# Performance work log

Hardware: AMD Instinct MI355X
Metric: run time of the kernel (lower is better)

The kernel has to match this reference:

```python
import jax, jax.numpy as jnp
import numpy as np

N, E, F_IN, D_HID, H, N_CLS = 50000, 800000, 128, 96, 8, 40
DH = D_HID // H  # 12
NEG_SLOPE = 0.2


def setup_inputs() -> dict:
    key = jax.random.key(0)
    ks = jax.random.split(key, 14)
    x = jax.random.normal(ks[0], (N, F_IN), dtype=jnp.float32)
    edge_src = jax.random.randint(ks[1], (E,), 0, N, dtype=jnp.int32)
    edge_dst = jax.random.randint(ks[2], (E,), 0, N, dtype=jnp.int32)
    s = 0.1  # keep attention logits in a stable range
    W0 = jax.random.normal(ks[3], (F_IN, D_HID), dtype=jnp.float32) * s
    as0 = jax.random.normal(ks[4], (H, DH), dtype=jnp.float32) * s
    ad0 = jax.random.normal(ks[5], (H, DH), dtype=jnp.float32) * s
    b0 = jnp.zeros((D_HID,), dtype=jnp.float32)
    W1 = jax.random.normal(ks[6], (D_HID, D_HID), dtype=jnp.float32) * s
    as1 = jax.random.normal(ks[7], (H, DH), dtype=jnp.float32) * s
    ad1 = jax.random.normal(ks[8], (H, DH), dtype=jnp.float32) * s
    b1 = jnp.zeros((D_HID,), dtype=jnp.float32)
    Wout = jax.random.normal(ks[9], (D_HID, N_CLS), dtype=jnp.float32) * s
    bout = jnp.zeros((N_CLS,), dtype=jnp.float32)
    return dict(x=x, edge_src=edge_src, edge_dst=edge_dst, W0=W0, as0=as0,
                ad0=ad0, b0=b0, W1=W1, as1=as1, ad1=ad1, b1=b1,
                Wout=Wout, bout=bout)


def _gat_conv(x, src, dst, W, a_src, a_dst, b):
    """PyG-style GATConv: per-head linear, edge attention, segment softmax, scatter-sum."""
    n = x.shape[0]
    h = (x @ W).reshape(n, H, DH)                       # [N, H, Dh]
    alpha_s = jnp.einsum('nhd,hd->nh', h, a_src)        # [N, H]
    alpha_d = jnp.einsum('nhd,hd->nh', h, a_dst)        # [N, H]
    e = alpha_s[src] + alpha_d[dst]                     # [E, H]
    e = jnp.where(e > 0, e, NEG_SLOPE * e)              # LeakyReLU(0.2)
    # numerically-stable segment softmax over edges grouped by destination
    m = jax.ops.segment_max(e, dst, num_segments=n)     # [N, H]
    m = jnp.where(jnp.isfinite(m), m, 0.0)
    p = jnp.exp(e - m[dst])                             # [E, H]
    z = jax.ops.segment_sum(p, dst, num_segments=n)     # [N, H]
    alpha = p / (z[dst] + 1e-16)                        # [E, H]
    msg = h[src] * alpha[:, :, None]                    # [E, H, Dh]
    out = jax.ops.segment_sum(msg, dst, num_segments=n) # [N, H, Dh]
    return out.reshape(n, H * DH) + b


def reference(x, edge_src, edge_dst, W0, as0, ad0, b0, W1, as1, ad1, b1, Wout, bout):
    src = edge_src.astype(jnp.int32)
    dst = edge_dst.astype(jnp.int32)
    h = _gat_conv(x, src, dst, W0, as0, ad0, b0)                 # input_fc (no activation)
    h = jax.nn.relu(_gat_conv(h, src, dst, W1, as1, ad1, b1))    # conv layer + ReLU (eval: no dropout)
    out = h @ Wout + bout
    return jax.nn.log_softmax(out, axis=1)
```

## Files before the change

kernel.cpp:

```cpp
#include <hip/hip_runtime.h>
#include <hip/hip_fp16.h>
#include <math.h>

#define N_NODES 50000
#define N_EDGES 800000
#define F_IN    128
#define D_HID   96
#define NHEAD   8
#define DH      12
#define N_CLS   40
#define NEG_SLOPE 0.2f

#define NPART   (N_NODES / 8)
#define CKS     64
#define CHK     (N_EDGES / CKS)
#define NHB     (8 * CKS)

#define GBM 64
#define NGB ((N_NODES + GBM - 1) / GBM)
#define WPAD 136

#define HALFN   (N_NODES / 2)
#define AGG_NPB 32
#define NAGGB   ((HALFN + AGG_NPB - 1) / AGG_NPB)

typedef _Float16 f16x8 __attribute__((ext_vector_type(8)));
typedef float    f32x4 __attribute__((ext_vector_type(4)));

__global__ __launch_bounds__(256) void pre_kernel(
    const float* __restrict__ W0, const float* __restrict__ W1,
    _Float16* __restrict__ wt0, _Float16* __restrict__ wt1)
{
    int b = blockIdx.x, t = threadIdx.x;
    if (b < 48) {
        int idx = b * 256 + t;
        int n = idx >> 7, k = idx & 127;
        wt0[idx] = (_Float16)W0[k * D_HID + n];
    } else {
        int idx = (b - 48) * 256 + t;
        int n = idx / 96, k = idx - n * 96;
        wt1[idx] = (_Float16)W1[k * D_HID + n];
    }
}

template<bool A16>
__device__ __forceinline__ void gemm_alpha_mfma_body(
    const void* __restrict__ Av, const _Float16* __restrict__ WT,
    const float* __restrict__ asrc, const float* __restrict__ adst,
    uint4* __restrict__ Hrec,
    int M, int K, int bid,
    _Float16 (*Wt)[WPAD], _Float16 (*Hl)[104], float* avl, float* adl)
{
    int tid  = threadIdx.x;
    int lane = tid & 63;
    int w    = tid >> 6;
    int n0   = bid * GBM;

    int cpr = K >> 3;
    int nch = 96 * cpr;
    for (int ch = tid; ch < nch; ch += 256) {
        int row = ch / cpr, off = (ch - row * cpr) << 3;
        *(f16x8*)&Wt[row][off] = *(const f16x8*)&WT[row * K + off];
    }
    if (tid < 96) { avl[tid] = asrc[tid]; adl[tid] = adst[tid]; }
    __syncthreads();

    int c  = lane & 15;
    int kg = lane >> 4;
    int arow = n0 + (w << 4) + c;
    int ar = arow < M ? arow : M - 1;

    f32x4 acc[6];
#pragma unroll
    for (int t = 0; t < 6; t++) acc[t] = (f32x4){0.f, 0.f, 0.f, 0.f};

    for (int k0 = 0; k0 < K; k0 += 32) {
        f16x8 av;
        if constexpr (A16) {
            const _Float16* ap = (const _Float16*)Av + (size_t)ar * K + (kg << 3);
            av = *(const f16x8*)(ap + k0);
        } else {
            const float* ap = (const float*)Av + (size_t)ar * K + (kg << 3);
            float4 a0 = *(const float4*)(ap + k0);
            float4 a1 = *(const float4*)(ap + k0 + 4);
            av[0] = (_Float16)a0.x; av[1] = (_Float16)a0.y;
            av[2] = (_Float16)a0.z; av[3] = (_Float16)a0.w;
            av[4] = (_Float16)a1.x; av[5] = (_Float16)a1.y;
            av[6] = (_Float16)a1.z; av[7] = (_Float16)a1.w;
        }
#pragma unroll
        for (int t = 0; t < 6; t++) {
            f16x8 bv = *(const f16x8*)&Wt[t * 16 + c][k0 + (kg << 3)];
            acc[t] = __builtin_amdgcn_mfma_f32_16x16x32_f16(av, bv, acc[t], 0, 0, 0);
        }
    }

    int rbase = (w << 4) + (kg << 2);
#pragma unroll
    for (int t = 0; t < 6; t++)
#pragma unroll
        for (int r = 0; r < 4; r++)
            Hl[rbase + r][t * 16 + c] = (_Float16)acc[t][r];
    __syncthreads();

    int row = tid >> 2, q = tid & 3;
    int gr = n0 + row;
    if (gr < M) {
        float s0 = 0.f, s1 = 0.f, d0 = 0.f, d1 = 0.f;
#pragma unroll
        for (int j = 0; j < 12; j++) {
            float f = (float)Hl[row][q * 24 + j];
            s0 += f * avl[q * 24 + j];
            d0 += f * adl[q * 24 + j];
        }
#pragma unroll
        for (int j = 12; j < 24; j++) {
            float f = (float)Hl[row][q * 24 + j];
            s1 += f * avl[q * 24 + j];
            d1 += f * adl[q * 24 + j];
        }
        const uint* hp = (const uint*)&Hl[row][q * 24];
        uint4* rec = Hrec + ((size_t)q * N_NODES + gr) * 4;
        rec[0] = make_uint4(__float_as_uint(s0), hp[0], hp[1], hp[2]);
        rec[1] = make_uint4(hp[3], hp[4], hp[5], __float_as_uint(d0));
        rec[2] = make_uint4(__float_as_uint(s1), hp[6], hp[7], hp[8]);
        rec[3] = make_uint4(hp[9], hp[10], hp[11], __float_as_uint(d1));
    }
}

__global__ __launch_bounds__(256) void hist_gemm_kernel(
    const int* __restrict__ edst, unsigned short* __restrict__ Hmat,
    const float* __restrict__ A, const _Float16* __restrict__ WT,
    const float* __restrict__ asrc, const float* __restrict__ adst,
    uint4* __restrict__ Hrec)
{
    __shared__ __align__(16) char smem[40448];
    if (blockIdx.x < NHB) {
        int* lh = (int*)smem;
        int g = blockIdx.x & 7, c = blockIdx.x >> 3;
        int lo = g * NPART;
        for (int i = threadIdx.x; i < NPART; i += 256) lh[i] = 0;
        __syncthreads();
        const int4* d4 = (const int4*)(edst + c * CHK);
        for (int i = threadIdx.x; i < CHK / 4; i += 256) {
            int4 dv = d4[i];
            int a = dv.x - lo, b = dv.y - lo, cc = dv.z - lo, dd = dv.w - lo;
            if ((unsigned)a  < (unsigned)NPART) atomicAdd(&lh[a], 1);
            if ((unsigned)b  < (unsigned)NPART) atomicAdd(&lh[b], 1);
            if ((unsigned)cc < (unsigned)NPART) atomicAdd(&lh[cc], 1);
            if ((unsigned)dd < (unsigned)NPART) atomicAdd(&lh[dd], 1);
        }
        __syncthreads();
        unsigned int* hrow = (unsigned int*)(Hmat + (size_t)c * N_NODES + lo);
        for (int i = threadIdx.x; i < NPART / 2; i += 256)
            hrow[i] = (unsigned)lh[2 * i] | ((unsigned)lh[2 * i + 1] << 16);
    } else {
        _Float16 (*Wt)[WPAD] = (_Float16(*)[WPAD])smem;
        _Float16 (*Hl)[104]  = (_Float16(*)[104])(smem + 26112);
        float* avl = (float*)(smem + 26112 + 13312);
        float* adl = avl + 96;
        gemm_alpha_mfma_body<false>(A, WT, asrc, adst, Hrec, N_NODES, F_IN,
                                    blockIdx.x - NHB, Wt, Hl, avl, adl);
    }
}

__global__ __launch_bounds__(256) void gemm_alpha_kernel(
    const _Float16* __restrict__ A, const _Float16* __restrict__ WT,
    const float* __restrict__ asrc, const float* __restrict__ adst,
    uint4* __restrict__ Hrec, int M, int K)
{
    __shared__ __align__(16) char smem[40448];
    _Float16 (*Wt)[WPAD] = (_Float16(*)[WPAD])smem;
    _Float16 (*Hl)[104]  = (_Float16(*)[104])(smem + 26112);
    float* avl = (float*)(smem + 26112 + 13312);
    float* adl = avl + 96;
    gemm_alpha_mfma_body<true>(A, WT, asrc, adst, Hrec, M, K, blockIdx.x,
                               Wt, Hl, avl, adl);
}

__global__ void scan1_kernel(const unsigned short* __restrict__ Hmat,
                             int* __restrict__ cnt, int* __restrict__ incl,
                             int* __restrict__ partials, int n) {
    __shared__ int sdata[256];
    int t = threadIdx.x;
    int base = blockIdx.x * 1024 + t * 4;
    int v[4] = {0, 0, 0, 0};
    if (base + 4 <= n) {
        for (int c = 0; c < CKS; c++) {
            ushort4 h = *(const ushort4*)&Hmat[(size_t)c * N_NODES + base];
            v[0] += h.x; v[1] += h.y; v[2] += h.z; v[3] += h.w;
        }
    } else if (base < n) {
        for (int c = 0; c < CKS; c++)
#pragma unroll
            for (int j = 0; j < 4; j++)
                if (base + j < n) v[j] += Hmat[(size_t)c * N_NODES + base + j];
    }
#pragma unroll
    for (int j = 0; j < 4; j++) if (base + j < n) cnt[base + j] = v[j];
    v[1] += v[0]; v[2] += v[1]; v[3] += v[2];
    sdata[t] = v[3];
    __syncthreads();
    for (int off = 1; off < 256; off <<= 1) {
        int x = (t >= off) ? sdata[t - off] : 0;
        __syncthreads();
        sdata[t] += x;
        __syncthreads();
    }
    int excl = sdata[t] - v[3];
#pragma unroll
    for (int j = 0; j < 4; j++) { int i = base + j; if (i < n) incl[i] = v[j] + excl; }
    if (t == 255) partials[blockIdx.x] = sdata[255];
}

__global__ void scan3_kernel(const int* __restrict__ cnt, const int* __restrict__ incl,
                             const int* __restrict__ partials,
                             const unsigned short* __restrict__ Hmat,
                             int* __restrict__ Bmat, int* __restrict__ rowptr,
                             int n, int nb) {
    int i = blockIdx.x * blockDim.x + threadIdx.x;
    if (i >= n) return;
    int myb = i >> 10;
    int psum = 0;
    for (int b = 0; b < nb; b++) psum += (b < myb) ? partials[b] : 0;
    int v = incl[i] + psum;
    rowptr[i + 1] = v;
    if (i == 0) rowptr[0] = 0;
    int running = v - cnt[i];
    for (int c = 0; c < CKS; c++) {
        Bmat[(size_t)c * N_NODES + i] = running;
        running += Hmat[(size_t)c * N_NODES + i];
    }
}

__global__ __launch_bounds__(256) void fill_kernel(
    const int* __restrict__ esrc, const int* __restrict__ edst,
    const int* __restrict__ Bmat, unsigned short* __restrict__ srclist)
{
    __shared__ int cur[NPART];
    int g = blockIdx.x & 7, c = blockIdx.x >> 3;
    int lo = g * NPART;
    const int* brow = Bmat + (size_t)c * N_NODES + lo;
    for (int i = threadIdx.x; i < NPART; i += 256) cur[i] = brow[i];
    __syncthreads();
    int base = c * CHK;
    const int4* d4 = (const int4*)(edst + base);
    const int4* s4 = (const int4*)(esrc + base);
    for (int i = threadIdx.x; i < CHK / 4; i += 256) {
        int4 dv = d4[i], sv = s4[i];
        int a = dv.x - lo, b = dv.y - lo, cc = dv.z - lo, dd = dv.w - lo;
        if ((unsigned)a < (unsigned)NPART) {
            int p = atomicAdd(&cur[a], 1); srclist[p] = (unsigned short)sv.x;
        }
        if ((unsigned)b < (unsigned)NPART) {
            int p = atomicAdd(&cur[b], 1); srclist[p] = (unsigned short)sv.y;
        }
        if ((unsigned)cc < (unsigned)NPART) {
            int p = atomicAdd(&cur[cc], 1); srclist[p] = (unsigned short)sv.z;
        }
        if ((unsigned)dd < (unsigned)NPART) {
            int p = atomicAdd(&cur[dd], 1); srclist[p] = (unsigned short)sv.w;
        }
    }
}

__device__ __forceinline__ void agg_rec(const uint4* __restrict__ rp, float ad,
                                        float& z, float* acc) {
    uint4 u0 = rp[0], u1 = rp[1];
    float e = __uint_as_float(u0.x) + ad;
    e = (e > 0.f) ? e : NEG_SLOPE * e;
    float p = __expf(e);
    z += p;
    float2 f0 = __half22float2(*(const __half2*)&u0.y);
    float2 f1 = __half22float2(*(const __half2*)&u0.z);
    float2 f2 = __half22float2(*(const __half2*)&u0.w);
    float2 f3 = __half22float2(*(const __half2*)&u1.x);
    float2 f4 = __half22float2(*(const __half2*)&u1.y);
    float2 f5 = __half22float2(*(const __half2*)&u1.z);
    acc[0] += p * f0.x; acc[1]  += p * f0.y;
    acc[2] += p * f1.x; acc[3]  += p * f1.y;
    acc[4] += p * f2.x; acc[5]  += p * f2.y;
    acc[6] += p * f3.x; acc[7]  += p * f3.y;
    acc[8] += p * f4.x; acc[9]  += p * f4.y;
    acc[10] += p * f5.x; acc[11] += p * f5.y;
}

__global__ __launch_bounds__(256) void gat_aggregate_kernel(
    const uint4* __restrict__ Hrec,
    const int* __restrict__ rowptr, const unsigned short* __restrict__ srclist,
    const float* __restrict__ bias,
    _Float16* __restrict__ outYh, float* __restrict__ outY, int mode)
{
    int s    = blockIdx.x & 7;
    int g    = s >> 1;
    int half = s & 1;
    int local = (blockIdx.x >> 3) * AGG_NPB + (threadIdx.x >> 3);
    if (local >= HALFN) return;
    int n   = half * HALFN + local;
    int l   = threadIdx.x & 7;
    int hh2 = l & 1;
    int j   = l >> 1;

    const uint4* gtab = Hrec + (size_t)g * N_NODES * 4;
    float ad = __uint_as_float(gtab[(size_t)n * 4 + hh2 * 2 + 1].w);

    int s0 = rowptr[n], s1 = rowptr[n + 1];
    float z = 0.f;
    float acc[12];
#pragma unroll
    for (int t = 0; t < 12; t++) acc[t] = 0.f;

    int i = s0 + j;
    for (; i + 4 < s1; i += 8) {
        int sa = srclist[i];
        int sb = srclist[i + 4];
        agg_rec(gtab + (size_t)sa * 4 + hh2 * 2, ad, z, acc);
        agg_rec(gtab + (size_t)sb * 4 + hh2 * 2, ad, z, acc);
    }
    if (i < s1) {
        int sa = srclist[i];
        agg_rec(gtab + (size_t)sa * 4 + hh2 * 2, ad, z, acc);
    }

#pragma unroll
    for (int m = 2; m <= 4; m <<= 1) {
        z += __shfl_xor(z, m, 64);
#pragma unroll
        for (int t = 0; t < 12; t++) acc[t] += __shfl_xor(acc[t], m, 64);
    }

    if (j == 0) {
        float inv = 1.f / (z + 1e-16f);
        const float* bp = bias + g * 24 + hh2 * 12;
        float o[12];
#pragma unroll
        for (int t = 0; t < 12; t++) o[t] = acc[t] * inv + bp[t];
        if (mode == 0) {
            uint ww[6];
#pragma unroll
            for (int t = 0; t < 6; t++) {
                __half2 hv = __floats2half2_rn(o[2 * t], o[2 * t + 1]);
                ww[t] = *(const uint*)&hv;
            }
            uint2* yp = (uint2*)(outYh + (size_t)n * D_HID + g * 24 + hh2 * 12);
            yp[0] = make_uint2(ww[0], ww[1]);
            yp[1] = make_uint2(ww[2], ww[3]);
            yp[2] = make_uint2(ww[4], ww[5]);
        } else {
#pragma unroll
            for (int t = 0; t < 12; t++) o[t] = fmaxf(o[t], 0.f);
            float4* op = (float4*)(outY + (size_t)n * D_HID + g * 24 + hh2 * 12);
            op[0] = make_float4(o[0], o[1], o[2], o[3]);
            op[1] = make_float4(o[4], o[5], o[6], o[7]);
            op[2] = make_float4(o[8], o[9], o[10], o[11]);
        }
    }
}

__global__ __launch_bounds__(256) void out_lsm_kernel(
    const float* __restrict__ X, const float* __restrict__ Wout,
    const float* __restrict__ bout, float* __restrict__ out)
{
    __shared__ float Ws[D_HID * N_CLS];
    __shared__ float bs[N_CLS];
    for (int i = threadIdx.x; i < D_HID * N_CLS; i += 256) Ws[i] = Wout[i];
    for (int i = threadIdx.x; i < N_CLS; i += 256) bs[i] = bout[i];
    __syncthreads();

    int n = blockIdx.x * blockDim.x + threadIdx.x;
    if (n >= N_NODES) return;

    float acc[N_CLS];
#pragma unroll
    for (int c = 0; c < N_CLS; c++) acc[c] = bs[c];

    const float4* xp = (const float4*)(X + (size_t)n * D_HID);
    for (int k4 = 0; k4 < D_HID / 4; k4++) {
        float4 xv = xp[k4];
        const float* wrow = &Ws[(k4 * 4) * N_CLS];
#pragma unroll
        for (int c4 = 0; c4 < N_CLS / 4; c4++) {
            float4 wa = *(const float4*)(wrow + c4 * 4);
            float4 wb = *(const float4*)(wrow + N_CLS + c4 * 4);
            float4 wc = *(const float4*)(wrow + 2 * N_CLS + c4 * 4);
            float4 wd = *(const float4*)(wrow + 3 * N_CLS + c4 * 4);
            acc[c4 * 4 + 0] += xv.x * wa.x + xv.y * wb.x + xv.z * wc.x + xv.w * wd.x;
            acc[c4 * 4 + 1] += xv.x * wa.y + xv.y * wb.y + xv.z * wc.y + xv.w * wd.y;
            acc[c4 * 4 + 2] += xv.x * wa.z + xv.y * wb.z + xv.z * wc.z + xv.w * wd.z;
            acc[c4 * 4 + 3] += xv.x * wa.w + xv.y * wb.w + xv.z * wc.w + xv.w * wd.w;
        }
    }

    float m = acc[0];
#pragma unroll
    for (int c = 1; c < N_CLS; c++) m = fmaxf(m, acc[c]);
    float s = 0.f;
#pragma unroll
    for (int c = 0; c < N_CLS; c++) s += __expf(acc[c] - m);
    float lg = __logf(s);

    float4* op = (float4*)(out + (size_t)n * N_CLS);
#pragma unroll
    for (int c4 = 0; c4 < N_CLS / 4; c4++) {
        op[c4] = make_float4(acc[c4 * 4 + 0] - m - lg, acc[c4 * 4 + 1] - m - lg,
                             acc[c4 * 4 + 2] - m - lg, acc[c4 * 4 + 3] - m - lg);
    }
}

extern "C" void kernel_launch(void* const* d_in, const int* in_sizes, int n_in,
                              void* d_out, int out_size, void* d_ws, size_t ws_size,
                              hipStream_t stream)
{
    const float* x    = (const float*)d_in[0];
    const int*   esrc = (const int*)d_in[1];
    const int*   edst = (const int*)d_in[2];
    const float* W0   = (const float*)d_in[3];
    const float* as0  = (const float*)d_in[4];
    const float* ad0  = (const float*)d_in[5];
    const float* b0   = (const float*)d_in[6];
    const float* W1   = (const float*)d_in[7];
    const float* as1  = (const float*)d_in[8];
    const float* ad1  = (const float*)d_in[9];
    const float* b1   = (const float*)d_in[10];
    const float* Wout = (const float*)d_in[11];
    const float* bout = (const float*)d_in[12];
    float* out = (float*)d_out;

    char* p = (char*)d_ws;
    float*    bufY  = (float*)p;    p += (size_t)N_NODES * D_HID * sizeof(float);
    _Float16* bufYh = (_Float16*)p; p += (size_t)N_NODES * D_HID * sizeof(_Float16);
    uint4*    Hrec  = (uint4*)p;    p += (size_t)4 * N_NODES * 64;
    int*   rowptr = (int*)p;   p += ((size_t)N_NODES + 16) * sizeof(int);
    int*   cnt    = (int*)p;   p += ((size_t)N_NODES + 16) * sizeof(int);
    int*   incl   = (int*)p;   p += ((size_t)N_NODES + 16) * sizeof(int);
    unsigned short* srclist = (unsigned short*)p; p += (size_t)N_EDGES * sizeof(unsigned short);
    int*   partials = (int*)p; p += 256;
    _Float16* wt0 = (_Float16*)p; p += (size_t)D_HID * F_IN * sizeof(_Float16);
    _Float16* wt1 = (_Float16*)p; p += (size_t)D_HID * D_HID * sizeof(_Float16);

    unsigned short* Hmat = (unsigned short*)bufYh;
    int*            Bmat = (int*)bufY;

    int nscan = (N_NODES + 1023) / 1024;

    pre_kernel<<<84, 256, 0, stream>>>(W0, W1, wt0, wt1);
    hist_gemm_kernel<<<NHB + NGB, 256, 0, stream>>>(
        edst, Hmat, x, wt0, as0, ad0, Hrec);
    scan1_kernel<<<nscan, 256, 0, stream>>>(Hmat, cnt, incl, partials, N_NODES);
    scan3_kernel<<<(N_NODES + 255) / 256, 256, 0, stream>>>(
        cnt, incl, partials, Hmat, Bmat, rowptr, N_NODES, nscan);
    fill_kernel<<<NHB, 256, 0, stream>>>(esrc, edst, Bmat, srclist);
    gat_aggregate_kernel<<<8 * NAGGB, 256, 0, stream>>>(
        Hrec, rowptr, srclist, b0, bufYh, bufY, 0);
    gemm_alpha_kernel<<<NGB, 256, 0, stream>>>(
        bufYh, wt1, as1, ad1, Hrec, N_NODES, D_HID);
    gat_aggregate_kernel<<<8 * NAGGB, 256, 0, stream>>>(
        Hrec, rowptr, srclist, b1, bufYh, bufY, 1);
    out_lsm_kernel<<<(N_NODES + 255) / 256, 256, 0, stream>>>(bufY, Wout, bout, out);
}
```

Baseline: 161.1 us.

## Drop weight pre-transpose kernel, shrink bucket offsets to 16-bit, unroll aggregation

Removes the separate pre_kernel launch; each GEMM block now converts and transposes the fp32 weights into shared memory itself. The per-chunk bucket offset matrix becomes 16-bit relative offsets added to rowptr in fill_kernel, which lets the cnt array and its writes go away and halves Bmat traffic. The aggregation loop is unrolled to four gathers per iteration for more memory-level parallelism. In exchange every GEMM block repeats the strided fp32 weight load and transpose, and the extra live gathers add register pressure.

```diff
diff --git a/kernel.cpp b/kernel.cpp
--- a/kernel.cpp
+++ b/kernel.cpp
@@ -27,25 +27,9 @@
 typedef _Float16 f16x8 __attribute__((ext_vector_type(8)));
 typedef float    f32x4 __attribute__((ext_vector_type(4)));
 
-__global__ __launch_bounds__(256) void pre_kernel(
-    const float* __restrict__ W0, const float* __restrict__ W1,
-    _Float16* __restrict__ wt0, _Float16* __restrict__ wt1)
-{
-    int b = blockIdx.x, t = threadIdx.x;
-    if (b < 48) {
-        int idx = b * 256 + t;
-        int n = idx >> 7, k = idx & 127;
-        wt0[idx] = (_Float16)W0[k * D_HID + n];
-    } else {
-        int idx = (b - 48) * 256 + t;
-        int n = idx / 96, k = idx - n * 96;
-        wt1[idx] = (_Float16)W1[k * D_HID + n];
-    }
-}
-
 template<bool A16>
 __device__ __forceinline__ void gemm_alpha_mfma_body(
-    const void* __restrict__ Av, const _Float16* __restrict__ WT,
+    const void* __restrict__ Av, const float* __restrict__ W,
     const float* __restrict__ asrc, const float* __restrict__ adst,
     uint4* __restrict__ Hrec,
     int M, int K, int bid,
@@ -56,11 +40,9 @@
     int w    = tid >> 6;
     int n0   = bid * GBM;
 
-    int cpr = K >> 3;
-    int nch = 96 * cpr;
-    for (int ch = tid; ch < nch; ch += 256) {
-        int row = ch / cpr, off = (ch - row * cpr) << 3;
-        *(f16x8*)&Wt[row][off] = *(const f16x8*)&WT[row * K + off];
+    for (int idx = tid; idx < K * 96; idx += 256) {
+        int k = idx / 96, n = idx - k * 96;
+        Wt[n][k] = (_Float16)W[idx];
     }
     if (tid < 96) { avl[tid] = asrc[tid]; adl[tid] = adst[tid]; }
     __syncthreads();
@@ -130,7 +112,7 @@
 
 __global__ __launch_bounds__(256) void hist_gemm_kernel(
     const int* __restrict__ edst, unsigned short* __restrict__ Hmat,
-    const float* __restrict__ A, const _Float16* __restrict__ WT,
+    const float* __restrict__ A, const float* __restrict__ W0,
     const float* __restrict__ asrc, const float* __restrict__ adst,
     uint4* __restrict__ Hrec)
 {
@@ -159,13 +141,13 @@
         _Float16 (*Hl)[104]  = (_Float16(*)[104])(smem + 26112);
         float* avl = (float*)(smem + 26112 + 13312);
         float* adl = avl + 96;
-        gemm_alpha_mfma_body<false>(A, WT, asrc, adst, Hrec, N_NODES, F_IN,
+        gemm_alpha_mfma_body<false>(A, W0, asrc, adst, Hrec, N_NODES, F_IN,
                                     blockIdx.x - NHB, Wt, Hl, avl, adl);
     }
 }
 
 __global__ __launch_bounds__(256) void gemm_alpha_kernel(
-    const _Float16* __restrict__ A, const _Float16* __restrict__ WT,
+    const _Float16* __restrict__ A, const float* __restrict__ W1,
     const float* __restrict__ asrc, const float* __restrict__ adst,
     uint4* __restrict__ Hrec, int M, int K)
 {
@@ -174,12 +156,12 @@
     _Float16 (*Hl)[104]  = (_Float16(*)[104])(smem + 26112);
     float* avl = (float*)(smem + 26112 + 13312);
     float* adl = avl + 96;
-    gemm_alpha_mfma_body<true>(A, WT, asrc, adst, Hrec, M, K, blockIdx.x,
+    gemm_alpha_mfma_body<true>(A, W1, asrc, adst, Hrec, M, K, blockIdx.x,
                                Wt, Hl, avl, adl);
 }
 
 __global__ void scan1_kernel(const unsigned short* __restrict__ Hmat,
-                             int* __restrict__ cnt, int* __restrict__ incl,
+                             int* __restrict__ incl,
                              int* __restrict__ partials, int n) {
     __shared__ int sdata[256];
     int t = threadIdx.x;
@@ -196,8 +178,6 @@
             for (int j = 0; j < 4; j++)
                 if (base + j < n) v[j] += Hmat[(size_t)c * N_NODES + base + j];
     }
-#pragma unroll
-    for (int j = 0; j < 4; j++) if (base + j < n) cnt[base + j] = v[j];
     v[1] += v[0]; v[2] += v[1]; v[3] += v[2];
     sdata[t] = v[3];
     __syncthreads();
@@ -213,10 +193,11 @@
     if (t == 255) partials[blockIdx.x] = sdata[255];
 }
 
-__global__ void scan3_kernel(const int* __restrict__ cnt, const int* __restrict__ incl,
+__global__ void scan3_kernel(const int* __restrict__ incl,
                              const int* __restrict__ partials,
                              const unsigned short* __restrict__ Hmat,
-                             int* __restrict__ Bmat, int* __restrict__ rowptr,
+                             unsigned short* __restrict__ Bmat16,
+                             int* __restrict__ rowptr,
                              int n, int nb) {
     int i = blockIdx.x * blockDim.x + threadIdx.x;
     if (i >= n) return;
@@ -226,22 +207,24 @@
     int v = incl[i] + psum;
     rowptr[i + 1] = v;
     if (i == 0) rowptr[0] = 0;
-    int running = v - cnt[i];
+    int running = 0;
     for (int c = 0; c < CKS; c++) {
-        Bmat[(size_t)c * N_NODES + i] = running;
+        Bmat16[(size_t)c * N_NODES + i] = (unsigned short)running;
         running += Hmat[(size_t)c * N_NODES + i];
     }
 }
 
 __global__ __launch_bounds__(256) void fill_kernel(
     const int* __restrict__ esrc, const int* __restrict__ edst,
-    const int* __restrict__ Bmat, unsigned short* __restrict__ srclist)
+    const int* __restrict__ rowptr, const unsigned short* __restrict__ Bmat16,
+    unsigned short* __restrict__ srclist)
 {
     __shared__ int cur[NPART];
     int g = blockIdx.x & 7, c = blockIdx.x >> 3;
     int lo = g * NPART;
-    const int* brow = Bmat + (size_t)c * N_NODES + lo;
-    for (int i = threadIdx.x; i < NPART; i += 256) cur[i] = brow[i];
+    const unsigned short* rrow = Bmat16 + (size_t)c * N_NODES + lo;
+    const int* rp = rowptr + lo;
+    for (int i = threadIdx.x; i < NPART; i += 256) cur[i] = rp[i] + rrow[i];
     __syncthreads();
     int base = c * CHK;
     const int4* d4 = (const int4*)(edst + base);
@@ -311,13 +294,17 @@
     for (int t = 0; t < 12; t++) acc[t] = 0.f;
 
     int i = s0 + j;
-    for (; i + 4 < s1; i += 8) {
+    for (; i + 12 < s1; i += 16) {
         int sa = srclist[i];
         int sb = srclist[i + 4];
+        int sc = srclist[i + 8];
+        int sd = srclist[i + 12];
         agg_rec(gtab + (size_t)sa * 4 + hh2 * 2, ad, z, acc);
         agg_rec(gtab + (size_t)sb * 4 + hh2 * 2, ad, z, acc);
-    }
-    if (i < s1) {
+        agg_rec(gtab + (size_t)sc * 4 + hh2 * 2, ad, z, acc);
+        agg_rec(gtab + (size_t)sd * 4 + hh2 * 2, ad, z, acc);
+    }
+    for (; i < s1; i += 4) {
         int sa = srclist[i];
         agg_rec(gtab + (size_t)sa * 4 + hh2 * 2, ad, z, acc);
     }
@@ -431,29 +418,25 @@
     _Float16* bufYh = (_Float16*)p; p += (size_t)N_NODES * D_HID * sizeof(_Float16);
     uint4*    Hrec  = (uint4*)p;    p += (size_t)4 * N_NODES * 64;
     int*   rowptr = (int*)p;   p += ((size_t)N_NODES + 16) * sizeof(int);
-    int*   cnt    = (int*)p;   p += ((size_t)N_NODES + 16) * sizeof(int);
     int*   incl   = (int*)p;   p += ((size_t)N_NODES + 16) * sizeof(int);
     unsigned short* srclist = (unsigned short*)p; p += (size_t)N_EDGES * sizeof(unsigned short);
     int*   partials = (int*)p; p += 256;
-    _Float16* wt0 = (_Float16*)p; p += (size_t)D_HID * F_IN * sizeof(_Float16);
-    _Float16* wt1 = (_Float16*)p; p += (size_t)D_HID * D_HID * sizeof(_Float16);
-
-    unsigned short* Hmat = (unsigned short*)bufYh;
-    int*            Bmat = (int*)bufY;
+
+    unsigned short* Hmat   = (unsigned short*)bufYh;
+    unsigned short* Bmat16 = (unsigned short*)bufY;
 
     int nscan = (N_NODES + 1023) / 1024;
 
-    pre_kernel<<<84, 256, 0, stream>>>(W0, W1, wt0, wt1);
     hist_gemm_kernel<<<NHB + NGB, 256, 0, stream>>>(
-        edst, Hmat, x, wt0, as0, ad0, Hrec);
-    scan1_kernel<<<nscan, 256, 0, stream>>>(Hmat, cnt, incl, partials, N_NODES);
+        edst, Hmat, x, W0, as0, ad0, Hrec);
+    scan1_kernel<<<nscan, 256, 0, stream>>>(Hmat, incl, partials, N_NODES);
     scan3_kernel<<<(N_NODES + 255) / 256, 256, 0, stream>>>(
-        cnt, incl, partials, Hmat, Bmat, rowptr, N_NODES, nscan);
-    fill_kernel<<<NHB, 256, 0, stream>>>(esrc, edst, Bmat, srclist);
+        incl, partials, Hmat, Bmat16, rowptr, N_NODES, nscan);
+    fill_kernel<<<NHB, 256, 0, stream>>>(esrc, edst, rowptr, Bmat16, srclist);
     gat_aggregate_kernel<<<8 * NAGGB, 256, 0, stream>>>(
         Hrec, rowptr, srclist, b0, bufYh, bufY, 0);
     gemm_alpha_kernel<<<NGB, 256, 0, stream>>>(
-        bufYh, wt1, as1, ad1, Hrec, N_NODES, D_HID);
+        bufYh, W1, as1, ad1, Hrec, N_NODES, D_HID);
     gat_aggregate_kernel<<<8 * NAGGB, 256, 0, stream>>>(
         Hrec, rowptr, srclist, b1, bufYh, bufY, 1);
     out_lsm_kernel<<<(N_NODES + 255) / 256, 256, 0, stream>>>(bufY, Wout, bout, out);
```

Measured after the change: 161.2 us. Within noise of the previous version (+0.0%).
